# Kernel tuning notes

Hardware: AMD Instinct MI355X
Metric: run time of the kernel (lower is better)

Reference implementation:

```python
import jax, jax.numpy as jnp
import numpy as np


def _lstm_dir(x, w_ih, w_hh, b_ih, b_hh, reverse):
    # x: [B, L, D]; w_ih: [4H, D]; w_hh: [4H, H]; PyTorch gate order i,f,g,o
    B = x.shape[0]
    H = w_hh.shape[1]
    h0 = jnp.zeros((B, H), x.dtype)

    def cell(carry, x_t):
        h, c = carry
        z = x_t @ w_ih.T + h @ w_hh.T + b_ih + b_hh
        i, f, g, o = jnp.split(z, 4, axis=-1)
        c = jax.nn.sigmoid(f) * c + jax.nn.sigmoid(i) * jnp.tanh(g)
        h = jax.nn.sigmoid(o) * jnp.tanh(c)
        return (h, c), h

    _, hs = jax.lax.scan(cell, (h0, h0), jnp.swapaxes(x, 0, 1), reverse=reverse)
    return jnp.swapaxes(hs, 0, 1)  # [B, L, H]


def setup_inputs() -> dict:
    key = jax.random.key(0)
    ks = jax.random.split(key, 16)
    B, L, V, D, H, E, A = 32, 128, 30000, 300, 128, 34, 36
    s = 0.05
    rn = lambda k, shape: jax.random.normal(k, shape, jnp.float32) * s
    return {
        "input_ids": jax.random.randint(ks[0], (B, L), 0, V),
        "emb": rn(ks[1], (V, D)),
        "w_ih_f": rn(ks[2], (4 * H, D)), "w_hh_f": rn(ks[3], (4 * H, H)),
        "b_ih_f": rn(ks[4], (4 * H,)), "b_hh_f": rn(ks[5], (4 * H,)),
        "w_ih_b": rn(ks[6], (4 * H, D)), "w_hh_b": rn(ks[7], (4 * H, H)),
        "b_ih_b": rn(ks[8], (4 * H,)), "b_hh_b": rn(ks[9], (4 * H,)),
        "event_w": rn(ks[10], (E, 2 * H)), "event_b": rn(ks[11], (E,)),
        "arg_w": rn(ks[12], (A, 4 * H + E - 1)), "arg_b": rn(ks[13], (A,)),
    }


def reference(input_ids, emb, w_ih_f, w_hh_f, b_ih_f, b_hh_f,
              w_ih_b, w_hh_b, b_ih_b, b_hh_b,
              event_w, event_b, arg_w, arg_b):
    # Eval mode: dropout is identity. No labels -> return (event_logits, arguments_logits).
    B, L = input_ids.shape
    E = event_b.shape[0]
    x = emb[input_ids]  # [B, L, D]
    h_f = _lstm_dir(x, w_ih_f, w_hh_f, b_ih_f, b_hh_f, False)
    h_b = _lstm_dir(x, w_ih_b, w_hh_b, b_ih_b, b_hh_b, True)
    hidden = jnp.concatenate([h_f, h_b], axis=-1)  # [B, L, 2H]
    col_range = jnp.arange(E - 1)
    g0 = jnp.zeros((B, L, E - 1), hidden.dtype)  # running g_trg_arg memory

    def step(g, h_i):  # h_i: [B, 2H] = trigger hidden state at timestep i
        ev_logit = h_i @ event_w.T + event_b  # [B, E]
        ev_pred = jnp.argmax(ev_logit, axis=-1)  # [B]
        trig = jnp.broadcast_to(h_i[:, None, :], hidden.shape)  # [B, L, 2H]
        ah = jnp.concatenate([hidden, trig, g], axis=-1)  # [B, L, 4H+E-1]
        arg_logit = ah @ arg_w.T + arg_b  # [B, L, A]
        arg_pred = jnp.argmax(arg_logit, axis=-1)  # [B, L]
        # Vectorized update_g_trg_arg: for batch items with ev_pred>0, set
        # column (ev_pred-1) to 1 wherever arg_pred>0, else keep previous value.
        mask_ev = ev_pred > 0  # [B]
        col = jnp.where(mask_ev, ev_pred - 1, 0)  # [B]
        onehot = (col[:, None] == col_range[None, :]) & mask_ev[:, None]  # [B, E-1]
        cond = onehot[:, None, :] & (arg_pred[:, :, None] > 0)  # [B, L, E-1]
        g = jnp.where(cond, jnp.ones((), g.dtype), g)
        return g, (ev_logit, arg_logit)

    _, (ev_logits, arg_logits) = jax.lax.scan(step, g0, jnp.swapaxes(hidden, 0, 1))
    event_logits = jnp.swapaxes(ev_logits, 0, 1)  # [B, L, E]
    arguments_logits = jnp.swapaxes(arg_logits, 0, 1)  # [B, L, L, A]
    return event_logits, arguments_logits
```

## Files before the change

### kernel.cpp

```cpp
#include <hip/hip_runtime.h>
#include <hip/hip_bf16.h>
#include <stdint.h>

#define B_  32
#define L_  128
#define D_  300
#define DP_ 304
#define H_  128
#define G_  512
#define E_  34
#define A_  36
#define M_  4096
#define NC_ 106
#define NCP 112
#define CH_ 8
#define NCH 16
#define LCH 8
#define NCHK (L_ / LCH)
#define BH_ 8

typedef float f2 __attribute__((ext_vector_type(2)));

__device__ __forceinline__ float sigf(float x){ return 1.0f / (1.0f + expf(-x)); }

__device__ __forceinline__ void bar_lds(){
    asm volatile("s_waitcnt lgkmcnt(0)" ::: "memory");
    __builtin_amdgcn_s_barrier();
    __builtin_amdgcn_sched_barrier(0);
}

__global__ void k_prep(const float* __restrict__ wihf, const float* __restrict__ wihb,
                       float* __restrict__ WT,
                       const float* __restrict__ evw, const float* __restrict__ evb,
                       const float* __restrict__ argw, const float* __restrict__ argb,
                       float* __restrict__ WcatT, float* __restrict__ biasv){
    int bid = blockIdx.x;
    int tid = threadIdx.x;
    if (bid < 2 * DP_){
        int d = bid / DP_, k = bid - d * DP_;
        const float* w = d ? wihb : wihf;
        WT[((size_t)d * DP_ + k) * G_ + tid] = (k < D_) ? w[(size_t)tid * D_ + k] : 0.0f;
    } else {
        int k = bid - 2 * DP_;
        int n = tid;
        if (n < NCP){
            float v = 0.0f;
            if (n < E_)       v = evw[(size_t)n * 256 + k];
            else if (n < 70)  v = argw[(size_t)(n - 34) * 545 + k];
            else if (n < NC_) v = argw[(size_t)(n - 70) * 545 + 256 + k];
            WcatT[(size_t)k * NCP + n] = v;
            if (k == 0){
                float bv = 0.0f;
                if (n < E_) bv = evb[n];
                else if (n < 70) bv = argb[n - 34];
                biasv[n] = bv;
            }
        }
    }
}

__launch_bounds__(256)
__global__ void k_gemm1(const int* __restrict__ ids, const float* __restrict__ emb,
                        const float* __restrict__ WT,
                        const float* __restrict__ bihf, const float* __restrict__ bhhf,
                        const float* __restrict__ bihb, const float* __restrict__ bhhb,
                        float* __restrict__ XW){
    __shared__ __align__(16) float xs[DP_][8];
    int d  = blockIdx.y;
    int m0 = blockIdx.x * 8;
    int tid = threadIdx.x;
    for (int idx = tid; idx < 8 * DP_; idx += 256){
        int r = idx / DP_, k = idx % DP_;
        int id = ids[m0 + r];
        xs[k][r] = (k < D_) ? emb[(size_t)id * D_ + k] : 0.0f;
    }
    __syncthreads();
    int n0 = tid, n1 = tid + 256;
    const float* w0 = WT + (size_t)d * DP_ * G_ + n0;
    const float* w1 = WT + (size_t)d * DP_ * G_ + n1;
    const float4* xs4 = (const float4*)xs;
    float acc0[8] = {}, acc1[8] = {};
    #pragma unroll 2
    for (int k = 0; k < D_; k++){
        float wv0 = w0[(size_t)k * G_];
        float wv1 = w1[(size_t)k * G_];
        float4 xA = xs4[k * 2], xB = xs4[k * 2 + 1];
        acc0[0] += xA.x * wv0; acc0[1] += xA.y * wv0;
        acc0[2] += xA.z * wv0; acc0[3] += xA.w * wv0;
        acc0[4] += xB.x * wv0; acc0[5] += xB.y * wv0;
        acc0[6] += xB.z * wv0; acc0[7] += xB.w * wv0;
        acc1[0] += xA.x * wv1; acc1[1] += xA.y * wv1;
        acc1[2] += xA.z * wv1; acc1[3] += xA.w * wv1;
        acc1[4] += xB.x * wv1; acc1[5] += xB.y * wv1;
        acc1[6] += xB.z * wv1; acc1[7] += xB.w * wv1;
    }
    float bias0 = d ? (bihb[n0] + bhhb[n0]) : (bihf[n0] + bhhf[n0]);
    float bias1 = d ? (bihb[n1] + bhhb[n1]) : (bihf[n1] + bhhf[n1]);
    for (int r = 0; r < 8; r++){
        XW[((size_t)d * M_ + m0 + r) * G_ + n0] = acc0[r] + bias0;
        XW[((size_t)d * M_ + m0 + r) * G_ + n1] = acc1[r] + bias1;
    }
}

#define PF(XR, CHI)                                                             \
{                                                                               \
    if ((CHI) < NCHK){                                                          \
        _Pragma("unroll")                                                       \
        for (int j = 0; j < LCH; j++){                                          \
            int s_ = (CHI) * LCH + j;                                           \
            int t_ = d ? (L_ - 1 - s_) : s_;                                    \
            XR[j] = xwn[(size_t)t_ * G_];                                       \
        }                                                                       \
    }                                                                           \
}

#define STEP8(XR, CHI)                                                          \
{                                                                               \
    _Pragma("unroll")                                                           \
    for (int j = 0; j < LCH; j++){                                              \
        int s_ = (CHI) * LCH + j;                                               \
        f2 a01 = {0.f, 0.f}, a23 = {0.f, 0.f};                                  \
        const float4* hc = (const float4*)hbuf;                                 \
        _Pragma("unroll")                                                       \
        for (int q = 0; q < 32; q++){                                           \
            float4 hv = hc[q];                                                  \
            f2 h01 = {hv.x, hv.y}, h23 = {hv.z, hv.w};                          \
            a01 = __builtin_elementwise_fma(wp[2*q],   h01, a01);               \
            a23 = __builtin_elementwise_fma(wp[2*q+1], h23, a23);               \
        }                                                                       \
        float z = XR[j] + ((a01.x + a01.y) + (a23.x + a23.y));                  \
        float v = gate_g ? tanhf(z) : sigf(z);                                  \
        zbuf[n] = v;                                                            \
        bar_lds();                                                              \
        if (n < H_){                                                            \
            float F = zbuf[H_ + n], G = zbuf[2*H_ + n], O = zbuf[3*H_ + n];     \
            c = F * c + v * G;                                                  \
            float h = O * tanhf(c);                                             \
            hbuf[n] = h;                                                        \
            hist[(size_t)(s_) * H_ + n] = h;                                    \
        }                                                                       \
        bar_lds();                                                              \
    }                                                                           \
}

__launch_bounds__(512, 2)
__global__ void k_lstm(const float* __restrict__ XW, const float* __restrict__ whhf,
                       const float* __restrict__ whhb, float* __restrict__ Hid){
    __shared__ __align__(16) float hbuf[H_];
    __shared__ float zbuf[G_];
    __shared__ __align__(16) float hist[L_ * H_];
    int bid = blockIdx.x;
    int d = bid >> 5, b = bid & 31;
    int n = threadIdx.x;
    bool gate_g = ((n >> 7) == 2);
    const float* whh = d ? whhb : whhf;
    const f2* wr2 = (const f2*)(whh + (size_t)n * H_);
    f2 wp[64];
    #pragma unroll
    for (int q = 0; q < 64; q++) wp[q] = wr2[q];
    float c = 0.0f;
    if (n < H_) hbuf[n] = 0.0f;
    __syncthreads();
    const float* xwn = XW + ((size_t)d * M_ + (size_t)b * L_) * G_ + n;
    float xA[LCH], xB[LCH];
    PF(xA, 0)
    #pragma unroll 1
    for (int cp = 0; cp < NCHK / 2; cp++){
        PF(xB, 2 * cp + 1)
        STEP8(xA, 2 * cp)
        PF(xA, 2 * cp + 2)
        STEP8(xB, 2 * cp + 1)
    }
    const float4* hist4 = (const float4*)hist;
    #pragma unroll
    for (int q = 0; q < 8; q++){
        int idx = n + q * 512;
        int sl = idx >> 5, n4 = idx & 31;
        int t_ = d ? (L_ - 1 - sl) : sl;
        *(float4*)(Hid + ((size_t)b * L_ + t_) * 256 + d * H_ + n4 * 4) =
            hist4[(size_t)sl * 32 + n4];
    }
}

__launch_bounds__(128)
__global__ void k_heads2(const float* __restrict__ Hid, const float* __restrict__ WcatT,
                         const float* __restrict__ biasv,
                         float* __restrict__ out0, float* __restrict__ Base,
                         float* __restrict__ T2, int* __restrict__ Evcol){
    __shared__ __align__(16) float hsT[256][BH_];
    __shared__ float outs[BH_][NCP];
    int m0 = blockIdx.x * BH_;
    int tid = threadIdx.x;
    #pragma unroll
    for (int r = 0; r < BH_; r++){
        hsT[tid][r]       = Hid[(size_t)(m0 + r) * 256 + tid];
        hsT[tid + 128][r] = Hid[(size_t)(m0 + r) * 256 + 128 + tid];
    }
    __syncthreads();
    if (tid < NC_){
        float acc[BH_] = {};
        const float* wc = WcatT + tid;
        for (int k = 0; k < 256; k++){
            float wv = wc[(size_t)k * NCP];
            float4 ha = *(const float4*)&hsT[k][0];
            float4 hb = *(const float4*)&hsT[k][4];
            acc[0] += ha.x * wv; acc[1] += ha.y * wv;
            acc[2] += ha.z * wv; acc[3] += ha.w * wv;
            acc[4] += hb.x * wv; acc[5] += hb.y * wv;
            acc[6] += hb.z * wv; acc[7] += hb.w * wv;
        }
        float bv = biasv[tid];
        #pragma unroll
        for (int r = 0; r < BH_; r++) outs[r][tid] = acc[r] + bv;
    }
    __syncthreads();
    for (int idx = tid; idx < BH_ * E_; idx += 128){
        int r = idx / E_, e = idx % E_;
        out0[(size_t)(m0 + r) * E_ + e] = outs[r][e];
    }
    for (int idx = tid; idx < BH_ * A_; idx += 128){
        int r = idx / A_, a = idx % A_;
        Base[(size_t)(m0 + r) * A_ + a] = outs[r][34 + a];
        T2[(size_t)(m0 + r) * A_ + a]   = outs[r][70 + a];
    }
    if (tid < BH_){
        float best = outs[tid][0]; int bi = 0;
        for (int e = 1; e < E_; e++){
            float v = outs[tid][e];
            if (v > best){ best = v; bi = e; }
        }
        Evcol[m0 + tid] = bi - 1;
    }
}

__launch_bounds__(128)
__global__ void k_scan1(const float* __restrict__ Base, const float* __restrict__ T2,
                        const int* __restrict__ Evcol, const float* __restrict__ argw,
                        float* __restrict__ Snap, uint64_t* __restrict__ MaskSnap){
    __shared__ __align__(16) float t2s[L_ * A_];
    __shared__ float wgs[33 * A_];
    __shared__ int   evc[L_];
    int b = blockIdx.x;
    int l = threadIdx.x;
    for (int idx = l; idx < L_ * A_ / 4; idx += 128)
        *(float4*)(t2s + idx * 4) = *(const float4*)(T2 + (size_t)b * L_ * A_ + idx * 4);
    for (int idx = l; idx < 33 * A_; idx += 128){
        int c = idx / A_, a = idx % A_;
        wgs[idx] = argw[(size_t)a * 545 + 512 + c];
    }
    evc[l] = Evcol[b * L_ + l];
    __syncthreads();
    float bg[A_];
    {
        const float* bp = Base + ((size_t)b * L_ + l) * A_;
        #pragma unroll
        for (int q = 0; q < 9; q++){
            float4 v = *(const float4*)(bp + 4 * q);
            bg[4*q] = v.x; bg[4*q+1] = v.y; bg[4*q+2] = v.z; bg[4*q+3] = v.w;
        }
    }
    uint64_t mask = 0;
    #pragma unroll 1
    for (int i = 0; i < L_; i++){
        if ((i & (CH_ - 1)) == 0){
            int ch = i >> 3;
            float* sp = Snap + (((size_t)b * NCH + ch) * L_ + l) * A_;
            #pragma unroll
            for (int q = 0; q < 9; q++){
                float4 v; v.x = bg[4*q]; v.y = bg[4*q+1]; v.z = bg[4*q+2]; v.w = bg[4*q+3];
                *(float4*)(sp + 4 * q) = v;
            }
            MaskSnap[((size_t)b * NCH + ch) * L_ + l] = mask;
        }
        float trv[A_];
        #pragma unroll
        for (int q = 0; q < 9; q++){
            float4 v = *(const float4*)(t2s + i * A_ + 4 * q);
            trv[4*q] = v.x; trv[4*q+1] = v.y; trv[4*q+2] = v.z; trv[4*q+3] = v.w;
        }
        float lg0 = bg[0] + trv[0];
        float m1  = bg[1] + trv[1];
        #pragma unroll
        for (int a = 2; a < A_; a++) m1 = fmaxf(m1, bg[a] + trv[a]);
        bool apos = m1 > lg0;
        int cc = evc[i];
        if (cc >= 0 && apos && !((mask >> cc) & 1ull)){
            mask |= 1ull << cc;
            const float* wc = wgs + cc * A_;
            #pragma unroll
            for (int a = 0; a < A_; a++) bg[a] += wc[a];
        }
    }
}

__launch_bounds__(128)
__global__ void k_scan2(const float* __restrict__ T2, const int* __restrict__ Evcol,
                        const float* __restrict__ argw,
                        const float* __restrict__ Snap, const uint64_t* __restrict__ MaskSnap,
                        float* __restrict__ argout){
    __shared__ __align__(16) float t2s[CH_ * A_];
    __shared__ float wgs[33 * A_];
    __shared__ int   evc[CH_];
    __shared__ float stg[L_ * 37];
    int ch = blockIdx.x;
    int b  = blockIdx.y;
    int l  = threadIdx.x;
    int i0 = ch * CH_;
    for (int idx = l; idx < CH_ * A_ / 4; idx += 128)
        *(float4*)(t2s + idx * 4) =
            *(const float4*)(T2 + ((size_t)b * L_ + i0) * A_ + idx * 4);
    for (int idx = l; idx < 33 * A_; idx += 128){
        int c = idx / A_, a = idx % A_;
        wgs[idx] = argw[(size_t)a * 545 + 512 + c];
    }
    if (l < CH_) evc[l] = Evcol[b * L_ + i0 + l];
    __syncthreads();
    float bg[A_];
    {
        const float* sp = Snap + (((size_t)b * NCH + ch) * L_ + l) * A_;
        #pragma unroll
        for (int q = 0; q < 9; q++){
            float4 v = *(const float4*)(sp + 4 * q);
            bg[4*q] = v.x; bg[4*q+1] = v.y; bg[4*q+2] = v.z; bg[4*q+3] = v.w;
        }
    }
    uint64_t mask = MaskSnap[((size_t)b * NCH + ch) * L_ + l];
    #pragma unroll 1
    for (int s = 0; s < CH_; s++){
        int i = i0 + s;
        float trv[A_];
        #pragma unroll
        for (int q = 0; q < 9; q++){
            float4 v = *(const float4*)(t2s + s * A_ + 4 * q);
            trv[4*q] = v.x; trv[4*q+1] = v.y; trv[4*q+2] = v.z; trv[4*q+3] = v.w;
        }
        float lg[A_];
        #pragma unroll
        for (int a = 0; a < A_; a++) lg[a] = bg[a] + trv[a];
        float m1 = lg[1];
        #pragma unroll
        for (int a = 2; a < A_; a++) m1 = fmaxf(m1, lg[a]);
        bool apos = m1 > lg[0];
        float* sr = stg + l * 37;
        #pragma unroll
        for (int a = 0; a < A_; a++) sr[a] = lg[a];
        int cc = evc[s];
        if (cc >= 0 && apos && !((mask >> cc) & 1ull)){
            mask |= 1ull << cc;
            const float* wc = wgs + cc * A_;
            #pragma unroll
            for (int a = 0; a < A_; a++) bg[a] += wc[a];
        }
        __syncthreads();
        float* op = argout + (((size_t)b * L_ + i) * L_) * A_;
        #pragma unroll
        for (int q = 0; q < 9; q++){
            int idx = l + q * 128;
            int row = idx / 9, c4 = idx % 9;
            const float* s0 = stg + row * 37 + c4 * 4;
            float4 v; v.x = s0[0]; v.y = s0[1]; v.z = s0[2]; v.w = s0[3];
            *(float4*)(op + (size_t)idx * 4) = v;
        }
        __syncthreads();
    }
}

extern "C" void kernel_launch(void* const* d_in, const int* in_sizes, int n_in,
                              void* d_out, int out_size, void* d_ws, size_t ws_size,
                              hipStream_t stream){
    const int*   ids  = (const int*)  d_in[0];
    const float* emb  = (const float*)d_in[1];
    const float* wihf = (const float*)d_in[2];
    const float* whhf = (const float*)d_in[3];
    const float* bihf = (const float*)d_in[4];
    const float* bhhf = (const float*)d_in[5];
    const float* wihb = (const float*)d_in[6];
    const float* whhb = (const float*)d_in[7];
    const float* bihb = (const float*)d_in[8];
    const float* bhhb = (const float*)d_in[9];
    const float* evw  = (const float*)d_in[10];
    const float* evb  = (const float*)d_in[11];
    const float* argw = (const float*)d_in[12];
    const float* argb = (const float*)d_in[13];

    float* out0   = (float*)d_out;
    float* argout = out0 + (size_t)M_ * E_;

    char* w = (char*)d_ws;
    float* WT    = (float*)w; w += (size_t)2 * DP_ * G_ * 4;
    float* XW    = (float*)w; w += (size_t)2 * M_ * G_ * 4;
    float* Hid   = (float*)w; w += (size_t)M_ * 256 * 4;
    float* WcatT = (float*)w; w += (size_t)256 * NCP * 4;
    float* biasv = (float*)w; w += (size_t)NCP * 4;
    float* Base  = (float*)w; w += (size_t)M_ * A_ * 4;
    float* T2    = (float*)w; w += (size_t)M_ * A_ * 4;
    int*   Evcol = (int*)w;   w += (size_t)M_ * 4;

    float*    Snap     = XW;
    uint64_t* MaskSnap = (uint64_t*)(XW + (size_t)B_ * NCH * L_ * A_);

    k_prep<<<2 * DP_ + 256, 512, 0, stream>>>(wihf, wihb, WT, evw, evb, argw, argb,
                                              WcatT, biasv);
    k_gemm1<<<dim3(M_ / 8, 2), 256, 0, stream>>>(ids, emb, WT, bihf, bhhf, bihb, bhhb, XW);
    k_lstm<<<64, 512, 0, stream>>>(XW, whhf, whhb, Hid);
    k_heads2<<<M_ / BH_, 128, 0, stream>>>(Hid, WcatT, biasv, out0, Base, T2, Evcol);
    k_scan1<<<B_, 128, 0, stream>>>(Base, T2, Evcol, argw, Snap, MaskSnap);
    k_scan2<<<dim3(NCH, B_), 128, 0, stream>>>(T2, Evcol, argw, Snap, MaskSnap, argout);
}
```

Baseline: 359.7 us.

## Split LSTM recurrent dot products across thread pairs and pair gates per thread

The recurrent LSTM step is reworked so each thread handles two gate rows (i/f paired with g/o) over half the hidden dimension. The two halves are combined with a lane shuffle. The i·tanh(g) product now stays in registers, so only the f and o activations go through shared memory. The hidden state is stored twice at offset positions so the two thread halves read separate copies and avoid bank conflicts. The aim is to shorten each serial timestep by cutting shared-memory reads and gate exchange per thread, at the cost of an extra shuffle and more register-held prefetch buffers.

After: 357.1 us. Within noise of the previous version (-0.7%).

```diff
diff --git a/kernel.cpp b/kernel.cpp
--- a/kernel.cpp
+++ b/kernel.cpp
@@ -102,42 +102,51 @@
     }
 }
 
-#define PF(XR, CHI)                                                             \
+#define PF(XR_A, XR_B, CHI)                                                     \
 {                                                                               \
     if ((CHI) < NCHK){                                                          \
         _Pragma("unroll")                                                       \
         for (int j = 0; j < LCH; j++){                                          \
             int s_ = (CHI) * LCH + j;                                           \
             int t_ = d ? (L_ - 1 - s_) : s_;                                    \
-            XR[j] = xwn[(size_t)t_ * G_];                                       \
+            XR_A[j] = xwA[(size_t)t_ * G_];                                     \
+            XR_B[j] = xwB[(size_t)t_ * G_];                                     \
         }                                                                       \
     }                                                                           \
 }
 
-#define STEP8(XR, CHI)                                                          \
+#define STEP8(XR_A, XR_B, CHI)                                                  \
 {                                                                               \
     _Pragma("unroll")                                                           \
     for (int j = 0; j < LCH; j++){                                              \
         int s_ = (CHI) * LCH + j;                                               \
-        f2 a01 = {0.f, 0.f}, a23 = {0.f, 0.f};                                  \
-        const float4* hc = (const float4*)hbuf;                                 \
+        f2 aA0 = {0.f, 0.f}, aA1 = {0.f, 0.f};                                  \
+        f2 aB0 = {0.f, 0.f}, aB1 = {0.f, 0.f};                                  \
         _Pragma("unroll")                                                       \
-        for (int q = 0; q < 32; q++){                                           \
+        for (int q = 0; q < 16; q++){                                           \
             float4 hv = hc[q];                                                  \
             f2 h01 = {hv.x, hv.y}, h23 = {hv.z, hv.w};                          \
-            a01 = __builtin_elementwise_fma(wp[2*q],   h01, a01);               \
-            a23 = __builtin_elementwise_fma(wp[2*q+1], h23, a23);               \
+            aA0 = __builtin_elementwise_fma(wA[2*q],   h01, aA0);               \
+            aA1 = __builtin_elementwise_fma(wA[2*q+1], h23, aA1);               \
+            aB0 = __builtin_elementwise_fma(wB[2*q],   h01, aB0);               \
+            aB1 = __builtin_elementwise_fma(wB[2*q+1], h23, aB1);               \
         }                                                                       \
-        float z = XR[j] + ((a01.x + a01.y) + (a23.x + a23.y));                  \
-        float v = gate_g ? tanhf(z) : sigf(z);                                  \
-        zbuf[n] = v;                                                            \
+        float pA = (aA0.x + aA0.y) + (aA1.x + aA1.y);                           \
+        float pB = (aB0.x + aB0.y) + (aB1.x + aB1.y);                           \
+        float oA = __shfl_xor(pA, 1);                                           \
+        float oB = __shfl_xor(pB, 1);                                           \
+        float zA = XR_A[j] + (pA + oA);                                         \
+        float zB = XR_B[j] + (pB + oB);                                         \
+        float vA = sigf(zA);                                                    \
+        float vB = glow ? tanhf(zB) : sigf(zB);                                 \
+        if (evenHi){ zbufF[u2] = vA; zbufO[u2] = vB; }                          \
         bar_lds();                                                              \
-        if (n < H_){                                                            \
-            float F = zbuf[H_ + n], G = zbuf[2*H_ + n], O = zbuf[3*H_ + n];     \
-            c = F * c + v * G;                                                  \
+        if (evenLo){                                                            \
+            float F = zbufF[u2], O = zbufO[u2];                                 \
+            c = F * c + vA * vB;                                                \
             float h = O * tanhf(c);                                             \
-            hbuf[n] = h;                                                        \
-            hist[(size_t)(s_) * H_ + n] = h;                                    \
+            hball[u2] = h; hball[132 + u2] = h;                                 \
+            hist[(size_t)(s_) * H_ + u2] = h;                                   \
         }                                                                       \
         bar_lds();                                                              \
     }                                                                           \
@@ -146,35 +155,44 @@
 __launch_bounds__(512, 2)
 __global__ void k_lstm(const float* __restrict__ XW, const float* __restrict__ whhf,
                        const float* __restrict__ whhb, float* __restrict__ Hid){
-    __shared__ __align__(16) float hbuf[H_];
-    __shared__ float zbuf[G_];
+    __shared__ __align__(16) float hball[260];
+    __shared__ float zbufF[H_], zbufO[H_];
     __shared__ __align__(16) float hist[L_ * H_];
     int bid = blockIdx.x;
     int d = bid >> 5, b = bid & 31;
-    int n = threadIdx.x;
-    bool gate_g = ((n >> 7) == 2);
+    int t = threadIdx.x;
+    int rowA = t >> 1;
+    int rowB = rowA + 256;
+    int hf   = t & 1;
+    bool glow   = (t < 256);
+    bool evenLo = (hf == 0) && (t < 256);
+    bool evenHi = (hf == 0) && (t >= 256);
+    int u2 = rowA & 127;
     const float* whh = d ? whhb : whhf;
-    const f2* wr2 = (const f2*)(whh + (size_t)n * H_);
-    f2 wp[64];
+    const f2* wrA = (const f2*)(whh + (size_t)rowA * H_ + hf * 64);
+    const f2* wrB = (const f2*)(whh + (size_t)rowB * H_ + hf * 64);
+    f2 wA[32], wB[32];
     #pragma unroll
-    for (int q = 0; q < 64; q++) wp[q] = wr2[q];
+    for (int q = 0; q < 32; q++){ wA[q] = wrA[q]; wB[q] = wrB[q]; }
+    const float4* hc = (const float4*)(hball + (hf ? 196 : 0));
     float c = 0.0f;
-    if (n < H_) hbuf[n] = 0.0f;
-    __syncthreads();
-    const float* xwn = XW + ((size_t)d * M_ + (size_t)b * L_) * G_ + n;
-    float xA[LCH], xB[LCH];
-    PF(xA, 0)
+    if (t < H_){ hball[t] = 0.0f; hball[132 + t] = 0.0f; }
+    __syncthreads();
+    const float* xwA = XW + ((size_t)d * M_ + (size_t)b * L_) * G_ + rowA;
+    const float* xwB = xwA + 256;
+    float xa[LCH], xb[LCH], ya[LCH], yb[LCH];
+    PF(xa, xb, 0)
     #pragma unroll 1
     for (int cp = 0; cp < NCHK / 2; cp++){
-        PF(xB, 2 * cp + 1)
-        STEP8(xA, 2 * cp)
-        PF(xA, 2 * cp + 2)
-        STEP8(xB, 2 * cp + 1)
+        PF(ya, yb, 2 * cp + 1)
+        STEP8(xa, xb, 2 * cp)
+        PF(xa, xb, 2 * cp + 2)
+        STEP8(ya, yb, 2 * cp + 1)
     }
     const float4* hist4 = (const float4*)hist;
     #pragma unroll
     for (int q = 0; q < 8; q++){
-        int idx = n + q * 512;
+        int idx = t + q * 512;
         int sl = idx >> 5, n4 = idx & 31;
         int t_ = d ? (L_ - 1 - sl) : sl;
         *(float4*)(Hid + ((size_t)b * L_ + t_) * 256 + d * H_ + n4 * 4) =
```
